# Optimization experiments

Measured on AMD Instinct MI355X. Metric: run time of the kernel, lower is better.

## Reference

```python
import jax, jax.numpy as jnp
import numpy as np

N_ATOMS = 50000
DEG = 16
N_EDGES = N_ATOMS * DEG
N_MOL = 1000
NA = 23  # NUMBER_ATOMIC_GRAPH_FEATURES
NB = 7   # NUMBER_BOND_GRAPH_FEATURES


def _sph(v):
    # e3nn-style real spherical harmonics, lmax=2, normalize=False, 'component' normalization
    x, y, z = v[:, 0], v[:, 1], v[:, 2]
    sh1 = jnp.sqrt(3.0) * jnp.stack([x, y, z], axis=-1)  # [E,3] (1o)
    sh2 = jnp.stack([
        jnp.sqrt(15.0) * x * y,
        jnp.sqrt(15.0) * y * z,
        (jnp.sqrt(5.0) / 2.0) * (2 * z * z - x * x - y * y),
        jnp.sqrt(15.0) * x * z,
        (jnp.sqrt(15.0) / 2.0) * (x * x - y * y),
    ], axis=-1)  # [E,5] (2e)
    return sh1, sh2


def setup_inputs() -> dict:
    key = jax.random.key(0)
    ks = jax.random.split(key, 10)
    positions = jax.random.normal(ks[0], (N_ATOMS, 3), jnp.float32)
    x = jax.random.normal(ks[1], (N_ATOMS, NA), jnp.float32)
    edge_attr = jax.random.uniform(ks[2], (N_EDGES, NB), jnp.float32)
    edge_src = jax.random.randint(ks[3], (N_EDGES,), 0, N_ATOMS)
    edge_dst = jnp.repeat(jnp.arange(N_ATOMS), DEG)  # every node has in-degree DEG (required by the module)
    batch = jnp.repeat(jnp.arange(N_MOL), N_ATOMS // N_MOL)
    # tp1: FullyConnectedTensorProduct(NAx0e, 7x0e+7x1o+7x2e -> 32x0e+12x1e+12x1o+8x2e+8x2o)
    # allowed paths: 0e*0e->0e (32), 0e*1o->1o (12), 0e*2e->2e (8); 1e/2o outputs have no path (zero)
    W1_0 = jax.random.normal(ks[4], (NA, NB, 32), jnp.float32)
    W1_1 = jax.random.normal(ks[5], (NA, NB, 12), jnp.float32)
    W1_2 = jax.random.normal(ks[6], (NA, NB, 8), jnp.float32)
    # tp2: paths into 0e: 0e*0e (32x7), 1o*1o (12x7), 2e*2e (8x7)
    W2_0 = jax.random.normal(ks[7], (32, NB, 1), jnp.float32)
    W2_1 = jax.random.normal(ks[8], (12, NB, 1), jnp.float32)
    W2_2 = jax.random.normal(ks[9], (8, NB, 1), jnp.float32)
    return {"positions": positions, "x": x, "edge_attr": edge_attr,
            "W1_0": W1_0, "W1_1": W1_1, "W1_2": W1_2,
            "W2_0": W2_0, "W2_1": W2_1, "W2_2": W2_2,
            "edge_src": edge_src, "edge_dst": edge_dst, "batch": batch}


def reference(positions, x, edge_attr, W1_0, W1_1, W1_2, W2_0, W2_1, W2_2, edge_src, edge_dst, batch):
    N = x.shape[0]
    E = edge_attr.shape[0]
    M = N_MOL
    vec = positions[edge_src] - positions[edge_dst]            # [E,3]
    sh1, sh2 = _sph(vec)
    # FullTensorProduct(7x0e, 0e+1o+2e): scalar block is edge_attr itself; l>0 blocks are outer products
    b1 = edge_attr[:, :, None] * sh1[:, None, :]               # [E,NB,3]
    b2 = edge_attr[:, :, None] * sh2[:, None, :]               # [E,NB,5]
    deg = jax.ops.segment_sum(jnp.ones((E,), positions.dtype), edge_dst, num_segments=N)
    inv_sqrt_deg = 1.0 / jnp.sqrt(deg)                          # all nodes have >=1 edge by construction
    # tp1 on gathered source atom scalars. Since in1 is all-scalar, the SH factor separates:
    t = x[edge_src][:, :, None] * edge_attr[:, None, :]         # [E,NA,NB]
    n1 = 1.0 / np.sqrt(NA * NB)                                 # fan-in normalization
    m0 = jnp.einsum('eab,abo->eo', t, W1_0) * n1                # [E,32] 0e
    m1 = (jnp.einsum('eab,abo->eo', t, W1_1) * n1)[:, :, None] * sh1[:, None, :]  # [E,12,3] 1o
    m2 = (jnp.einsum('eab,abo->eo', t, W1_2) * n1)[:, :, None] * sh2[:, None, :]  # [E,8,5] 2e
    # (tp1's 12x1e and 8x2o outputs are structurally zero and have no path into tp2's 0e output -> dropped)
    s0 = jax.ops.segment_sum(m0, edge_dst, num_segments=N) * inv_sqrt_deg[:, None]
    s1 = jax.ops.segment_sum(m1, edge_dst, num_segments=N) * inv_sqrt_deg[:, None, None]
    s2 = jax.ops.segment_sum(m2, edge_dst, num_segments=N) * inv_sqrt_deg[:, None, None]
    # tp2 -> single 0e; l x l -> 0 contraction is inner product / sqrt(2l+1)
    e0 = jnp.einsum('ea,eb,ab->e', s0[edge_src], edge_attr, W2_0[:, :, 0]) / np.sqrt(32 * NB)
    e1 = jnp.einsum('eam,ebm,ab->e', s1[edge_src], b1, W2_1[:, :, 0]) / (np.sqrt(12 * NB) * np.sqrt(3.0))
    e2 = jnp.einsum('eam,ebm,ab->e', s2[edge_src], b2, W2_2[:, :, 0]) / (np.sqrt(8 * NB) * np.sqrt(5.0))
    edge_out = (e0 + e1 + e2)[:, None]                          # [E,1]
    node_out = jax.ops.segment_sum(edge_out, edge_dst, num_segments=N) * inv_sqrt_deg[:, None]
    apm = jax.ops.segment_sum(jnp.ones((N,), positions.dtype), batch, num_segments=M)
    acc = jax.ops.segment_sum(node_out, batch, num_segments=M)  # [M,1]
    return acc / jnp.sqrt(apm)[:, None]
```

## Files before the change

kernel.cpp:

```cpp
#include <hip/hip_runtime.h>
#include <hip/hip_bf16.h>

#define N_ATOMS 50000
#define DEG 16
#define N_MOL 1000
#define NA 23
#define NB 7
#define O0 32
#define O1 12
#define O2 8
#define OT 52
#define SROW 128
#define NPW 4
#define WFRAG_N 1792


typedef __attribute__((ext_vector_type(8))) short short8;
typedef __attribute__((ext_vector_type(4))) float floatx4;

__device__ __forceinline__ unsigned short bfbits(float f) {
    unsigned u = __float_as_uint(f);
    u += 0x7FFFu + ((u >> 16) & 1u);
    return (unsigned short)(u >> 16);
}
__device__ __forceinline__ float bf_lo(unsigned u) { return __uint_as_float(u << 16); }
__device__ __forceinline__ float bf_hi(unsigned u) { return __uint_as_float(u & 0xFFFF0000u); }
__device__ __forceinline__ float wred4(float v) {
    v += __shfl_xor(v, 16, 64); v += __shfl_xor(v, 32, 64); return v;
}

__global__ void k_prep(const float* __restrict__ W1_0, const float* __restrict__ W1_1,
                       const float* __restrict__ W1_2, unsigned short* __restrict__ Wfrag,
                       float* __restrict__ out) {
    int idx = blockIdx.x * 256 + threadIdx.x;
    if (idx < N_MOL) out[idx] = 0.0f;
    if (idx >= WFRAG_N * 8) return;
    int j    = idx & 7;
    int lane = (idx >> 3) & 63;
    int st   = idx >> 9;
    int s = st >> 2, t = st & 3;
    int a = (lane >> 4) * 8 + j, o = t * 16 + (lane & 15);
    float val = 0.f;
    if (a < NA && o < OT) {
        const float n1 = 0.07881104062391006f;
        if (o < O0)           val = W1_0[(a * NB + s) * O0 + o] * n1;
        else if (o < O0 + O1) val = W1_1[(a * NB + s) * O1 + (o - O0)] * n1;
        else                  val = W1_2[(a * NB + s) * O2 + (o - O0 - O1)] * n1;
    }
    Wfrag[idx] = bfbits(val);
}

__global__ __launch_bounds__(256, 5) void k2_s(const float* __restrict__ pos,
        const float* __restrict__ x, const float* __restrict__ edge_attr,
        const int* __restrict__ edge_src, const unsigned short* __restrict__ Wfrag,
        unsigned short* __restrict__ sbuf) {
    __shared__ short8 wfrag[WFRAG_N];
    __shared__ float hbuf[4][16][8];
    const int tid  = threadIdx.x;
    const int wid  = tid >> 6;
    const int lane = tid & 63;
    const int lcol = lane & 15;
    const int quad = lane >> 4;

    {
        uint4* dst = (uint4*)wfrag;
        const uint4* src4 = (const uint4*)Wfrag;
        for (int i = tid; i < WFRAG_N; i += 256) dst[i] = src4[i];
    }
    __syncthreads();

    const int wgid = __builtin_amdgcn_readfirstlane(blockIdx.x * 4 + wid);
    const int base = wgid * NPW;
    if (base >= N_ATOMS) return;

    float (*hb)[8] = hbuf[wid];
    const float s3 = 1.7320508075688772f, s15 = 3.872983346207417f;
    const float s5h = 1.118033988749895f, s15h = 1.9364916731037085f;

    auto clampn = [&](int i) { int nn = base + i; return nn < N_ATOMS ? nn : N_ATOMS - 1; };
    int s0v = edge_src[clampn(0) * DEG + lcol];
    int s1v = edge_src[clampn(1) * DEG + lcol];
    float x0[8], e0v[NB];
    float p0x, p0y, p0z;
    #pragma unroll
    for (int j = 0; j < 8; j++) { int a = quad * 8 + j; x0[j] = (a < NA) ? x[s0v * NA + a] : 0.f; }
    {
        const float* p = edge_attr + ((size_t)clampn(0) * DEG + lcol) * NB;
        #pragma unroll
        for (int b = 0; b < NB; b++) e0v[b] = p[b];
    }
    p0x = pos[s0v * 3 + 0]; p0y = pos[s0v * 3 + 1]; p0z = pos[s0v * 3 + 2];

    #pragma unroll 1
    for (int i = 0; i < NPW; i++) {
        const int n = base + i;
        if (n >= N_ATOMS) break;
        int s2v = edge_src[clampn(i + 2 < NPW ? i + 2 : i) * DEG + lcol];
        float x1[8], e1v[NB], p1x, p1y, p1z;
        #pragma unroll
        for (int j = 0; j < 8; j++) { int a = quad * 8 + j; x1[j] = (a < NA) ? x[s1v * NA + a] : 0.f; }
        {
            const float* p = edge_attr + ((size_t)clampn(i + 1 < NPW ? i + 1 : i) * DEG + lcol) * NB;
            #pragma unroll
            for (int b = 0; b < NB; b++) e1v[b] = p[b];
        }
        p1x = pos[s1v * 3 + 0]; p1y = pos[s1v * 3 + 1]; p1z = pos[s1v * 3 + 2];

        const float pdx = pos[n * 3 + 0], pdy = pos[n * 3 + 1], pdz = pos[n * 3 + 2];
        if (lane < 16) {
            const float vx = p0x - pdx, vy = p0y - pdy, vz = p0z - pdz;
            hb[lane][0] = s3 * vx;  hb[lane][1] = s3 * vy;  hb[lane][2] = s3 * vz;
            hb[lane][3] = s15 * vx * vy;
            hb[lane][4] = s15 * vy * vz;
            hb[lane][5] = s5h * (2.f * vz * vz - vx * vx - vy * vy);
            hb[lane][6] = s15 * vx * vz;
            hb[lane][7] = s15h * (vx * vx - vy * vy);
        }
        floatx4 acc0 = {0.f,0.f,0.f,0.f}, acc1 = {0.f,0.f,0.f,0.f};
        floatx4 acc2 = {0.f,0.f,0.f,0.f}, acc3 = {0.f,0.f,0.f,0.f};
        #pragma unroll
        for (int s = 0; s < 7; s++) {
            const float eb = e0v[s];
            union { short8 v; unsigned u[4]; } af;
            #pragma unroll
            for (int j = 0; j < 8; j += 2) {
                float2 pr; pr.x = x0[j] * eb; pr.y = x0[j + 1] * eb;
                __hip_bfloat162 bb = __float22bfloat162_rn(pr);
                af.u[j >> 1] = *(unsigned*)&bb;
            }
            acc0 = __builtin_amdgcn_mfma_f32_16x16x32_bf16(af.v, wfrag[(s*4+0)*64 + lane], acc0, 0, 0, 0);
            acc1 = __builtin_amdgcn_mfma_f32_16x16x32_bf16(af.v, wfrag[(s*4+1)*64 + lane], acc1, 0, 0, 0);
            acc2 = __builtin_amdgcn_mfma_f32_16x16x32_bf16(af.v, wfrag[(s*4+2)*64 + lane], acc2, 0, 0, 0);
            acc3 = __builtin_amdgcn_mfma_f32_16x16x32_bf16(af.v, wfrag[(s*4+3)*64 + lane], acc3, 0, 0, 0);
        }
        float4 hA[4], hB[4];
        #pragma unroll
        for (int r = 0; r < 4; r++) {
            int e = quad * 4 + r;
            hA[r] = *(const float4*)&hb[e][0];
            hB[r] = *(const float4*)&hb[e][4];
        }
        const float q = 0.25f;
        unsigned short* sr = sbuf + (size_t)n * SROW;
        float v0 = wred4(acc0[0] + acc0[1] + acc0[2] + acc0[3]);
        float v1 = wred4(acc1[0] + acc1[1] + acc1[2] + acc1[3]);
        if (quad == 0) { sr[lcol] = bfbits(v0 * q); sr[16 + lcol] = bfbits(v1 * q); }
        if (lcol < 12) {
            float t0 = 0.f, t1 = 0.f, t2 = 0.f;
            #pragma unroll
            for (int r = 0; r < 4; r++) {
                float m = acc2[r];
                t0 += m * hA[r].x; t1 += m * hA[r].y; t2 += m * hA[r].z;
            }
            t0 = wred4(t0); t1 = wred4(t1); t2 = wred4(t2);
            if (quad == 0) {
                sr[32 + lcol] = bfbits(t0 * q);
                sr[44 + lcol] = bfbits(t1 * q);
                sr[56 + lcol] = bfbits(t2 * q);
            }
        } else {
            int a = lcol - 12;
            float t0 = 0.f, t1 = 0.f, t2 = 0.f, t3 = 0.f, t4 = 0.f;
            #pragma unroll
            for (int r = 0; r < 4; r++) {
                float m = acc2[r];
                t0 += m * hA[r].w; t1 += m * hB[r].x; t2 += m * hB[r].y;
                t3 += m * hB[r].z; t4 += m * hB[r].w;
            }
            t0 = wred4(t0); t1 = wred4(t1); t2 = wred4(t2); t3 = wred4(t3); t4 = wred4(t4);
            if (quad == 0) {
                sr[68 + a] = bfbits(t0 * q); sr[76 + a] = bfbits(t1 * q);
                sr[84 + a] = bfbits(t2 * q); sr[92 + a] = bfbits(t3 * q);
                sr[100 + a] = bfbits(t4 * q);
            }
        }
        if (lcol < 4) {
            int a = lcol + 4;
            float t0 = 0.f, t1 = 0.f, t2 = 0.f, t3 = 0.f, t4 = 0.f;
            #pragma unroll
            for (int r = 0; r < 4; r++) {
                float m = acc3[r];
                t0 += m * hA[r].w; t1 += m * hB[r].x; t2 += m * hB[r].y;
                t3 += m * hB[r].z; t4 += m * hB[r].w;
            }
            t0 = wred4(t0); t1 = wred4(t1); t2 = wred4(t2); t3 = wred4(t3); t4 = wred4(t4);
            if (quad == 0) {
                sr[68 + a] = bfbits(t0 * q); sr[76 + a] = bfbits(t1 * q);
                sr[84 + a] = bfbits(t2 * q); sr[92 + a] = bfbits(t3 * q);
                sr[100 + a] = bfbits(t4 * q);
            }
        }
        s0v = s1v; s1v = s2v;
        #pragma unroll
        for (int j = 0; j < 8; j++) x0[j] = x1[j];
        #pragma unroll
        for (int b = 0; b < NB; b++) e0v[b] = e1v[b];
        p0x = p1x; p0y = p1y; p0z = p1z;
    }
}

__global__ __launch_bounds__(256, 7) void k3_fused(const float* __restrict__ pos,
        const float* __restrict__ edge_attr, const int* __restrict__ edge_src,
        const unsigned short* __restrict__ sbuf,
        const float* __restrict__ W2_0, const float* __restrict__ W2_1,
        const float* __restrict__ W2_2, float* __restrict__ out) {
    __shared__ float ea_t[4][4][16][8];
    __shared__ float hbf[4][4][192];
    const int tid  = threadIdx.x;
    const int wid  = tid >> 6;
    const int lane = tid & 63;
    const int q    = lane >> 4;
    const int e    = lane & 15;
    const int base = __builtin_amdgcn_readfirstlane(blockIdx.x * 4 + wid) * 4;

    const float c0 = 0.06681531047810609f;
    const float c1 = 0.06299407883487121f;
    const float c2 = 0.05976143046671968f;
    int code = 0, aA = 0, aB = 0, valid = 1;
    const float* Wb = W2_0; float norm = c0;
    const int j = lane;
    if (j < 16)      { code = 0; aA = 2 * j;   aB = aA + 1; Wb = W2_0; norm = c0; }
    else if (j < 34) { int g = (j - 16) / 6, r = (j - 16) - 6 * g;
                       code = 1 + g; aA = 2 * r; aB = aA + 1; Wb = W2_1; norm = c1; }
    else if (j < 54) { int g = (j - 34) >> 2, r = (j - 34) & 3;
                       code = 4 + g; aA = 2 * r; aB = aA + 1; Wb = W2_2; norm = c2; }
    else             { valid = 0; }
    float wA[NB], wB[NB];
    #pragma unroll
    for (int b = 0; b < NB; b++) {
        wA[b] = valid ? Wb[aA * NB + b] * norm : 0.f;
        wB[b] = valid ? Wb[aB * NB + b] * norm : 0.f;
    }
    const int jj = valid ? j : 0;

    {
        const int nq = base + q;
        const int sE = edge_src[nq * DEG + e];
        const float* eap = edge_attr + ((size_t)nq * DEG + e) * NB;
        float ev[8];
        #pragma unroll
        for (int b = 0; b < NB; b++) ev[b] = eap[b];
        ev[7] = 0.f;
        const float vx = pos[sE * 3 + 0] - pos[nq * 3 + 0];
        const float vy = pos[sE * 3 + 1] - pos[nq * 3 + 1];
        const float vz = pos[sE * 3 + 2] - pos[nq * 3 + 2];
        float* ed = &ea_t[wid][q][e][0];
        *(float4*)(ed)     = *(float4*)&ev[0];
        *(float4*)(ed + 4) = *(float4*)&ev[4];
        const float s3 = 1.7320508075688772f, s15 = 3.872983346207417f;
        const float s5h = 1.118033988749895f, s15h = 1.9364916731037085f;
        float* hr = &hbf[wid][q][e * 12];
        hr[0] = 1.0f;
        hr[1] = s3 * vx; hr[2] = s3 * vy; hr[3] = s3 * vz;
        hr[4] = s15 * vx * vy;
        hr[5] = s15 * vy * vz;
        hr[6] = s5h * (2.f * vz * vz - vx * vx - vy * vy);
        hr[7] = s15 * vx * vz;
        hr[8] = s15h * (vx * vx - vy * vy);
    }

    const int* srcp = edge_src + (size_t)base * DEG;
    unsigned g0[DEG], g1[DEG];
    #pragma unroll
    for (int k = 0; k < DEG; k++) {
        int s = __builtin_amdgcn_readfirstlane(srcp[k]);
        g0[k] = *(const unsigned*)(sbuf + (size_t)s * SROW + 2 * jj);
    }
    #pragma unroll
    for (int i = 0; i < 4; i++) {
        if (i + 1 < 4) {
            #pragma unroll
            for (int k = 0; k < DEG; k++) {
                int s = __builtin_amdgcn_readfirstlane(srcp[(i + 1) * DEG + k]);
                g1[k] = *(const unsigned*)(sbuf + (size_t)s * SROW + 2 * jj);
            }
        }
        const float* hw = &hbf[wid][i][0];
        float acc = 0.f;
        #pragma unroll
        for (int k = 0; k < DEG; k++) {
            const float4 eA = *(const float4*)&ea_t[wid][i][k][0];
            const float4 eB = *(const float4*)&ea_t[wid][i][k][4];
            const float f = hw[k * 12 + code];
            float we0 = eA.x * wA[0] + eA.y * wA[1] + eA.z * wA[2] + eA.w * wA[3]
                      + eB.x * wA[4] + eB.y * wA[5] + eB.z * wA[6];
            float we1 = eA.x * wB[0] + eA.y * wB[1] + eA.z * wB[2] + eA.w * wB[3]
                      + eB.x * wB[4] + eB.y * wB[5] + eB.z * wB[6];
            acc += f * (bf_lo(g0[k]) * we0 + bf_hi(g0[k]) * we1);
        }
        acc = valid ? acc : 0.f;
        #pragma unroll
        for (int off = 32; off >= 1; off >>= 1) acc += __shfl_xor(acc, off, 64);
        if (lane == 0)
            atomicAdd(out + ((base + i) / 50), acc * 0.035355339059327376f);
        #pragma unroll
        for (int k = 0; k < DEG; k++) g0[k] = g1[k];
    }
}

extern "C" void kernel_launch(void* const* d_in, const int* in_sizes, int n_in,
                              void* d_out, int out_size, void* d_ws, size_t ws_size,
                              hipStream_t stream) {
    const float* pos  = (const float*)d_in[0];
    const float* x    = (const float*)d_in[1];
    const float* ea   = (const float*)d_in[2];
    const float* W1_0 = (const float*)d_in[3];
    const float* W1_1 = (const float*)d_in[4];
    const float* W1_2 = (const float*)d_in[5];
    const float* W2_0 = (const float*)d_in[6];
    const float* W2_1 = (const float*)d_in[7];
    const float* W2_2 = (const float*)d_in[8];
    const int*   esrc = (const int*)d_in[9];
    float* out = (float*)d_out;

    unsigned short* Wfrag = (unsigned short*)d_ws;
    unsigned short* sbuf  = (unsigned short*)((char*)d_ws + 32768);

    hipLaunchKernelGGL(k_prep, dim3(WFRAG_N * 8 / 256), dim3(256), 0, stream,
                       W1_0, W1_1, W1_2, Wfrag, out);
    hipLaunchKernelGGL(k2_s, dim3((N_ATOMS / NPW + 3) / 4), dim3(256), 0, stream,
                       pos, x, ea, esrc, Wfrag, sbuf);
    hipLaunchKernelGGL(k3_fused, dim3(N_ATOMS / 16), dim3(256), 0, stream,
                       pos, ea, esrc, sbuf, W2_0, W2_1, W2_2, out);
}
```

Baseline: 208.1 us.

## Pre-pack x to padded bf16 rows and positions to float4 for vector gathers

The prep kernel now also converts x into 32-wide bf16 rows and pads positions into float4, so k2_s gathers each neighbor's features with a single 16-byte load and positions with one load instead of scalar strided loads. k3_fused also reads the float4 positions. It shrinks the per-edge LDS stride for the harmonic buffer from 12 to 10 and raises the occupancy hint. The cost is an extra prep pass over all atoms with additional workspace writes, plus bf16 rounding of x before the product with edge_attr.

```diff
diff --git a/kernel.cpp b/kernel.cpp
--- a/kernel.cpp
+++ b/kernel.cpp
@@ -14,7 +14,6 @@
 #define NPW 4
 #define WFRAG_N 1792
 
-
 typedef __attribute__((ext_vector_type(8))) short short8;
 typedef __attribute__((ext_vector_type(4))) float floatx4;
 
@@ -30,28 +29,41 @@
 }
 
 __global__ void k_prep(const float* __restrict__ W1_0, const float* __restrict__ W1_1,
-                       const float* __restrict__ W1_2, unsigned short* __restrict__ Wfrag,
+                       const float* __restrict__ W1_2, const float* __restrict__ x,
+                       const float* __restrict__ pos,
+                       unsigned short* __restrict__ Wfrag,
+                       unsigned short* __restrict__ x_bf, float4* __restrict__ pos4,
                        float* __restrict__ out) {
     int idx = blockIdx.x * 256 + threadIdx.x;
     if (idx < N_MOL) out[idx] = 0.0f;
-    if (idx >= WFRAG_N * 8) return;
-    int j    = idx & 7;
-    int lane = (idx >> 3) & 63;
-    int st   = idx >> 9;
-    int s = st >> 2, t = st & 3;
-    int a = (lane >> 4) * 8 + j, o = t * 16 + (lane & 15);
-    float val = 0.f;
-    if (a < NA && o < OT) {
-        const float n1 = 0.07881104062391006f;
-        if (o < O0)           val = W1_0[(a * NB + s) * O0 + o] * n1;
-        else if (o < O0 + O1) val = W1_1[(a * NB + s) * O1 + (o - O0)] * n1;
-        else                  val = W1_2[(a * NB + s) * O2 + (o - O0 - O1)] * n1;
-    }
-    Wfrag[idx] = bfbits(val);
-}
-
-__global__ __launch_bounds__(256, 5) void k2_s(const float* __restrict__ pos,
-        const float* __restrict__ x, const float* __restrict__ edge_attr,
+    if (idx < WFRAG_N * 8) {
+        int j    = idx & 7;
+        int lane = (idx >> 3) & 63;
+        int st   = idx >> 9;
+        int s = st >> 2, t = st & 3;
+        int a = (lane >> 4) * 8 + j, o = t * 16 + (lane & 15);
+        float val = 0.f;
+        if (a < NA && o < OT) {
+            const float n1 = 0.07881104062391006f;
+            if (o < O0)           val = W1_0[(a * NB + s) * O0 + o] * n1;
+            else if (o < O0 + O1) val = W1_1[(a * NB + s) * O1 + (o - O0)] * n1;
+            else                  val = W1_2[(a * NB + s) * O2 + (o - O0 - O1)] * n1;
+        }
+        Wfrag[idx] = bfbits(val);
+    }
+    if (idx < N_ATOMS) {
+        float4 p; p.x = pos[idx * 3 + 0]; p.y = pos[idx * 3 + 1];
+        p.z = pos[idx * 3 + 2]; p.w = 0.f;
+        pos4[idx] = p;
+    }
+    if (idx < N_ATOMS * 32) {
+        int n = idx >> 5, a = idx & 31;
+        x_bf[idx] = bfbits((a < NA) ? x[n * NA + a] : 0.f);
+    }
+}
+
+__global__ __launch_bounds__(256, 5) void k2_s(const float4* __restrict__ pos4,
+        const unsigned short* __restrict__ x_bf, const float* __restrict__ edge_attr,
         const int* __restrict__ edge_src, const unsigned short* __restrict__ Wfrag,
         unsigned short* __restrict__ sbuf) {
     __shared__ short8 wfrag[WFRAG_N];
@@ -80,35 +92,37 @@
     auto clampn = [&](int i) { int nn = base + i; return nn < N_ATOMS ? nn : N_ATOMS - 1; };
     int s0v = edge_src[clampn(0) * DEG + lcol];
     int s1v = edge_src[clampn(1) * DEG + lcol];
-    float x0[8], e0v[NB];
-    float p0x, p0y, p0z;
-    #pragma unroll
-    for (int j = 0; j < 8; j++) { int a = quad * 8 + j; x0[j] = (a < NA) ? x[s0v * NA + a] : 0.f; }
+    uint4 xu0 = *(const uint4*)(x_bf + s0v * 32 + quad * 8);
+    float4 pp0 = pos4[s0v];
+    float e0v[NB];
     {
         const float* p = edge_attr + ((size_t)clampn(0) * DEG + lcol) * NB;
         #pragma unroll
         for (int b = 0; b < NB; b++) e0v[b] = p[b];
     }
-    p0x = pos[s0v * 3 + 0]; p0y = pos[s0v * 3 + 1]; p0z = pos[s0v * 3 + 2];
 
     #pragma unroll 1
     for (int i = 0; i < NPW; i++) {
         const int n = base + i;
         if (n >= N_ATOMS) break;
         int s2v = edge_src[clampn(i + 2 < NPW ? i + 2 : i) * DEG + lcol];
-        float x1[8], e1v[NB], p1x, p1y, p1z;
-        #pragma unroll
-        for (int j = 0; j < 8; j++) { int a = quad * 8 + j; x1[j] = (a < NA) ? x[s1v * NA + a] : 0.f; }
+        uint4 xu1 = *(const uint4*)(x_bf + s1v * 32 + quad * 8);
+        float4 pp1 = pos4[s1v];
+        float e1v[NB];
         {
             const float* p = edge_attr + ((size_t)clampn(i + 1 < NPW ? i + 1 : i) * DEG + lcol) * NB;
             #pragma unroll
             for (int b = 0; b < NB; b++) e1v[b] = p[b];
         }
-        p1x = pos[s1v * 3 + 0]; p1y = pos[s1v * 3 + 1]; p1z = pos[s1v * 3 + 2];
-
-        const float pdx = pos[n * 3 + 0], pdy = pos[n * 3 + 1], pdz = pos[n * 3 + 2];
+        float xf[8];
+        xf[0] = bf_lo(xu0.x); xf[1] = bf_hi(xu0.x);
+        xf[2] = bf_lo(xu0.y); xf[3] = bf_hi(xu0.y);
+        xf[4] = bf_lo(xu0.z); xf[5] = bf_hi(xu0.z);
+        xf[6] = bf_lo(xu0.w); xf[7] = bf_hi(xu0.w);
+
+        const float4 pd = pos4[n];
         if (lane < 16) {
-            const float vx = p0x - pdx, vy = p0y - pdy, vz = p0z - pdz;
+            const float vx = pp0.x - pd.x, vy = pp0.y - pd.y, vz = pp0.z - pd.z;
             hb[lane][0] = s3 * vx;  hb[lane][1] = s3 * vy;  hb[lane][2] = s3 * vz;
             hb[lane][3] = s15 * vx * vy;
             hb[lane][4] = s15 * vy * vz;
@@ -124,7 +138,7 @@
             union { short8 v; unsigned u[4]; } af;
             #pragma unroll
             for (int j = 0; j < 8; j += 2) {
-                float2 pr; pr.x = x0[j] * eb; pr.y = x0[j + 1] * eb;
+                float2 pr; pr.x = xf[j] * eb; pr.y = xf[j + 1] * eb;
                 __hip_bfloat162 bb = __float22bfloat162_rn(pr);
                 af.u[j >> 1] = *(unsigned*)&bb;
             }
@@ -191,21 +205,19 @@
             }
         }
         s0v = s1v; s1v = s2v;
-        #pragma unroll
-        for (int j = 0; j < 8; j++) x0[j] = x1[j];
+        xu0 = xu1; pp0 = pp1;
         #pragma unroll
         for (int b = 0; b < NB; b++) e0v[b] = e1v[b];
-        p0x = p1x; p0y = p1y; p0z = p1z;
-    }
-}
-
-__global__ __launch_bounds__(256, 7) void k3_fused(const float* __restrict__ pos,
+    }
+}
+
+__global__ __launch_bounds__(256, 8) void k3_fused(const float4* __restrict__ pos4,
         const float* __restrict__ edge_attr, const int* __restrict__ edge_src,
         const unsigned short* __restrict__ sbuf,
         const float* __restrict__ W2_0, const float* __restrict__ W2_1,
         const float* __restrict__ W2_2, float* __restrict__ out) {
     __shared__ float ea_t[4][4][16][8];
-    __shared__ float hbf[4][4][192];
+    __shared__ float hbf[4][4][161];
     const int tid  = threadIdx.x;
     const int wid  = tid >> 6;
     const int lane = tid & 63;
@@ -241,15 +253,15 @@
         #pragma unroll
         for (int b = 0; b < NB; b++) ev[b] = eap[b];
         ev[7] = 0.f;
-        const float vx = pos[sE * 3 + 0] - pos[nq * 3 + 0];
-        const float vy = pos[sE * 3 + 1] - pos[nq * 3 + 1];
-        const float vz = pos[sE * 3 + 2] - pos[nq * 3 + 2];
+        const float4 ps = pos4[sE];
+        const float4 pd = pos4[nq];
+        const float vx = ps.x - pd.x, vy = ps.y - pd.y, vz = ps.z - pd.z;
         float* ed = &ea_t[wid][q][e][0];
         *(float4*)(ed)     = *(float4*)&ev[0];
         *(float4*)(ed + 4) = *(float4*)&ev[4];
         const float s3 = 1.7320508075688772f, s15 = 3.872983346207417f;
         const float s5h = 1.118033988749895f, s15h = 1.9364916731037085f;
-        float* hr = &hbf[wid][q][e * 12];
+        float* hr = &hbf[wid][q][e * 10];
         hr[0] = 1.0f;
         hr[1] = s3 * vx; hr[2] = s3 * vy; hr[3] = s3 * vz;
         hr[4] = s15 * vx * vy;
@@ -281,7 +293,7 @@
         for (int k = 0; k < DEG; k++) {
             const float4 eA = *(const float4*)&ea_t[wid][i][k][0];
             const float4 eB = *(const float4*)&ea_t[wid][i][k][4];
-            const float f = hw[k * 12 + code];
+            const float f = hw[k * 10 + code];
             float we0 = eA.x * wA[0] + eA.y * wA[1] + eA.z * wA[2] + eA.w * wA[3]
                       + eB.x * wA[4] + eB.y * wA[5] + eB.z * wA[6];
             float we1 = eA.x * wB[0] + eA.y * wB[1] + eA.z * wB[2] + eA.w * wB[3]
@@ -313,13 +325,16 @@
     const int*   esrc = (const int*)d_in[9];
     float* out = (float*)d_out;
 
-    unsigned short* Wfrag = (unsigned short*)d_ws;
-    unsigned short* sbuf  = (unsigned short*)((char*)d_ws + 32768);
-
-    hipLaunchKernelGGL(k_prep, dim3(WFRAG_N * 8 / 256), dim3(256), 0, stream,
-                       W1_0, W1_1, W1_2, Wfrag, out);
+    char* ws = (char*)d_ws;
+    unsigned short* Wfrag = (unsigned short*)ws;
+    unsigned short* sbuf  = (unsigned short*)(ws + 32768);
+    unsigned short* x_bf  = (unsigned short*)(ws + 32768 + 12800000);
+    float4*         pos4  = (float4*)(ws + 32768 + 12800000 + 3200000);
+
+    hipLaunchKernelGGL(k_prep, dim3((N_ATOMS * 32 + 255) / 256), dim3(256), 0, stream,
+                       W1_0, W1_1, W1_2, x, pos, Wfrag, x_bf, pos4, out);
     hipLaunchKernelGGL(k2_s, dim3((N_ATOMS / NPW + 3) / 4), dim3(256), 0, stream,
-                       pos, x, ea, esrc, Wfrag, sbuf);
+                       pos4, x_bf, ea, esrc, Wfrag, sbuf);
     hipLaunchKernelGGL(k3_fused, dim3(N_ATOMS / 16), dim3(256), 0, stream,
-                       pos, ea, esrc, sbuf, W2_0, W2_1, W2_2, out);
-}
+                       pos4, ea, esrc, sbuf, W2_0, W2_1, W2_2, out);
+}
```

Result: no change. 208.1 us (-0.0%).
